# Kernel optimization log

Hardware: AMD Instinct MI355X
Metric: run time of the kernel (lower is better)

## Reference

```python
import jax, jax.numpy as jnp
import numpy as np

H = 12  # num_heads (init kwarg)


def setup_inputs() -> dict:
    key = jax.random.key(0)
    ks = jax.random.split(key, 9)
    B, S, D, M = 2, 1025, 768, 4
    hw = S - 1
    x = jax.random.normal(ks[0], (B, S, D), dtype=jnp.float32)
    masks = jax.random.randint(ks[1], (B, M, hw), 0, 2, dtype=jnp.int32)
    init = lambda k: jax.random.normal(k, (D, D), dtype=jnp.float32) * 0.02
    return {
        'x': x, 'masks': masks,
        'Wq': init(ks[2]), 'bq': jnp.zeros((D,), jnp.float32),
        'Wk': init(ks[3]), 'bk': jnp.zeros((D,), jnp.float32),
        'Wv': init(ks[4]), 'bv': jnp.zeros((D,), jnp.float32),
    }


def reference(x, masks, Wq, bq, Wk, bk, Wv, bv):
    B, S, D = x.shape
    hd = D // H
    scale = 1.0 / jnp.sqrt(jnp.asarray(hd, x.dtype))

    def heads(t):  # (B,S,D) -> (B,H,S,hd)
        return t.reshape(B, S, H, hd).transpose(0, 2, 1, 3)

    q = heads(x @ Wq.T + bq)
    k = heads(x @ Wk.T + bk)
    v = heads(x @ Wv.T + bv)

    scores_ori = jnp.einsum('bhqd,bhkd->bhqk', q, k) * scale  # (B,H,S,S)
    attn = jax.nn.softmax(scores_ori, axis=-1)  # dropout is identity at eval
    h = jnp.einsum('bhqk,bhkd->bhqd', attn, v)
    h = h.transpose(0, 2, 1, 3).reshape(B, S, D)

    # ---- mask-expanded attention (torch.no_grad branch) ----
    Mk, hw = masks.shape[1], masks.shape[2]
    m = masks.astype(x.dtype)  # (B,M,hw)
    # pad: position 0 (CLS) gets 0, positions 1..hw get the mask
    new_masks = jnp.pad(m, ((0, 0), (0, 0), (1, S - 1 - hw)))  # (B,M,S)
    bias = -10000.0 * (1.0 - new_masks)  # additive mask bias
    new_scores = scores_ori[:, None] + bias[:, :, None, None, :]  # (B,M,H,S,S)
    new_attn = jax.nn.softmax(new_scores, axis=-1)
    new_h = jnp.einsum('bmhqk,bhkd->bmhqd', new_attn, v)  # v repeated per mask
    new_h = new_h.transpose(0, 1, 3, 2, 4).reshape(B * Mk, S, D)

    img_idx = jnp.repeat(jnp.arange(B), Mk)  # [0]*M + [1]*M + ...
    new_x = jnp.broadcast_to(x[:, None], (B, Mk, S, D)).reshape(B * Mk, S, D)
    return (h, new_h, img_idx, new_x)
```

## Files before the change

### kernel.cpp

```cpp
#include <hip/hip_runtime.h>

typedef float f32x4 __attribute__((ext_vector_type(4)));
typedef short s16x8 __attribute__((ext_vector_type(8)));

constexpr int B  = 2;
constexpr int S  = 1025;
constexpr int D  = 768;
constexpr int DD = D * D;
constexpr int H  = 12;
constexpr int NM = 4;
constexpr int ROWS = B * S;
constexpr int BSD  = B * S * D;
constexpr int KPAD = 1088;
constexpr int NHB  = B * H;
constexpr int NQT  = 65;
constexpr int NKT  = 17;
constexpr int NV5  = 5;
constexpr int NATT = NHB * NQT;
constexpr int NCPY = 512;
constexpr int OUT_NEWH_OFF = BSD;
constexpr int OUT_IDX_OFF  = BSD + NM * BSD;
constexpr int OUT_NEWX_OFF = OUT_IDX_OFF + B * NM;

#define QSCALE 0.18033688011112042f

constexpr size_t QF_SZ = (size_t)NHB * NQT * 2 * 512;
constexpr size_t KF_SZ = (size_t)NHB * NKT * 4 * 2 * 512;
constexpr size_t VF_SZ = KF_SZ;

__device__ __forceinline__ unsigned short f2bf(float f) {
    unsigned u = __builtin_bit_cast(unsigned, f);
    u += 0x7FFF + ((u >> 16) & 1);
    return (unsigned short)(u >> 16);
}

__device__ __forceinline__ void gll16(const void* g, void* l) {
    __builtin_amdgcn_global_load_lds(
        (const __attribute__((address_space(1))) void*)g,
        (__attribute__((address_space(3))) void*)l, 16, 0, 0);
}

__global__ __launch_bounds__(256) void conv_kernel(
    const float* __restrict__ x, const float* __restrict__ Wq,
    const float* __restrict__ Wk, const float* __restrict__ Wv,
    const int* __restrict__ masks,
    unsigned short* __restrict__ xb, unsigned short* __restrict__ Wb,
    unsigned short* __restrict__ Mmb,
    unsigned short* __restrict__ Qf, unsigned short* __restrict__ Kf,
    unsigned short* __restrict__ Vf)
{
    constexpr int NX8 = BSD / 8;
    constexpr int NW8 = DD / 8;
    constexpr int TOT = NX8 + 3 * NW8;
    const int stride = gridDim.x * 256;
    const int tid = blockIdx.x * 256 + threadIdx.x;
    for (int c = tid; c < TOT; c += stride) {
        const float* src;
        unsigned short* dst;
        if (c < NX8) { src = x + (size_t)c * 8; dst = xb + (size_t)c * 8; }
        else {
            const int cc = c - NX8;
            const int mt = cc / NW8;
            const int rr = cc - mt * NW8;
            src = ((mt == 0) ? Wq : (mt == 1) ? Wk : Wv) + (size_t)rr * 8;
            dst = Wb + (size_t)mt * DD + (size_t)rr * 8;
        }
        const float4 a = *(const float4*)src;
        const float4 b2 = *(const float4*)(src + 4);
        s16x8 v;
        v[0] = (short)f2bf(a.x);  v[1] = (short)f2bf(a.y);
        v[2] = (short)f2bf(a.z);  v[3] = (short)f2bf(a.w);
        v[4] = (short)f2bf(b2.x); v[5] = (short)f2bf(b2.y);
        v[6] = (short)f2bf(b2.z); v[7] = (short)f2bf(b2.w);
        *(s16x8*)dst = v;
    }
    if (tid < B * NV5 * KPAD) {
        const int k    = tid % KPAD;
        const int rest = tid / KPAD;
        const int vv   = rest % NV5;
        const int bb   = rest / NV5;
        unsigned short m;
        if (vv == 0) m = (k < S) ? 0xFFFFu : 0u;
        else m = (k >= 1 && k < S &&
                  masks[(size_t)(bb * NM + vv - 1) * (S - 1) + k - 1]) ? 0xFFFFu : 0u;
        Mmb[tid] = m;
    }
    constexpr int KZ = NHB * 8 * 512;
    for (int i = tid; i < KZ; i += stride) {
        const int hb = i >> 12, off = i & 4095;
        Kf[(((size_t)(hb * NKT + NKT - 1)) << 12) + off] = 0;
        Vf[(((size_t)(hb * NKT + NKT - 1)) << 12) + off] = 0;
    }
    constexpr int QZ = NHB * 2 * 512;
    for (int i = tid; i < QZ; i += stride) {
        const int hb = i >> 10, off = i & 1023;
        Qf[(((size_t)(hb * NQT + NQT - 1) * 2) << 9) + off] = 0;
    }
}

__global__ __launch_bounds__(256, 2) void qkv_mfma_kernel(
    const unsigned short* __restrict__ xb, const unsigned short* __restrict__ Wb,
    const float* __restrict__ bq, const float* __restrict__ bk,
    const float* __restrict__ bv,
    unsigned short* __restrict__ Qf, unsigned short* __restrict__ Kf,
    unsigned short* __restrict__ Vf)
{
    __shared__ __align__(16) unsigned short Xs[2][64 * 64];
    __shared__ __align__(16) unsigned short Wl[2][64 * 64];

    const int t = threadIdx.x;
    const int row0 = blockIdx.x * 64;
    const int yy = blockIdx.y;
    const int mt = yy / 12;
    const int col0 = (yy % 12) * 64;
    const float* bias = (mt == 0) ? bq : (mt == 1) ? bk : bv;
    const unsigned short* Wsrc = Wb + (size_t)mt * DD;

    const int w = t >> 6, l = t & 63, lq = l & 15, grp = l >> 4;

    auto stage = [&](int buf, int k0) {
        #pragma unroll
        for (int i = 0; i < 2; ++i) {
            const int slot = i * 256 + t;
            const int r = slot >> 3, cl = slot & 7;
            const int cg = cl ^ (r & 7);
            int row = row0 + r; if (row > ROWS - 1) row = ROWS - 1;
            gll16(xb + (size_t)row * D + k0 + cg * 8, &Xs[buf][slot * 8]);
            gll16(Wsrc + (size_t)(col0 + r) * D + k0 + cg * 8, &Wl[buf][slot * 8]);
        }
    };

    f32x4 acc[4] = {};
    stage(0, 0);

    for (int ks = 0; ks < 12; ++ks) {
        const int cur = ks & 1;
        __syncthreads();
        if (ks + 1 < 12) stage(cur ^ 1, (ks + 1) * 64);

        s16x8 a[2];
        const int xr = w * 16 + lq;
        #pragma unroll
        for (int kh = 0; kh < 2; ++kh)
            a[kh] = *(const s16x8*)&Xs[cur][xr * 64 + (((kh * 4 + grp) ^ (xr & 7)) * 8)];
        #pragma unroll
        for (int nt = 0; nt < 4; ++nt) {
            const int wr = nt * 16 + lq;
            #pragma unroll
            for (int kh = 0; kh < 2; ++kh) {
                s16x8 bfr = *(const s16x8*)&Wl[cur][wr * 64 + (((kh * 4 + grp) ^ (wr & 7)) * 8)];
                acc[nt] = __builtin_amdgcn_mfma_f32_16x16x32_bf16(a[kh], bfr, acc[nt], 0, 0, 0);
            }
        }
    }

    #pragma unroll
    for (int nt = 0; nt < 4; ++nt) {
        const int col = col0 + nt * 16 + lq;
        const float bv_ = bias[col];
        #pragma unroll
        for (int r = 0; r < 4; ++r) {
            const int row = row0 + w * 16 + grp * 4 + r;
            if (row >= ROWS) continue;
            const float raw = acc[nt][r] + bv_;
            const int bb = (row >= S) ? 1 : 0;
            const int s  = row - bb * S;
            const int hb2 = bb * H + (col >> 6);
            const int d   = col & 63;
            if (mt == 0) {
                const size_t idx = (((size_t)(hb2 * NQT + (s >> 4)) * 2 + (d >> 5)) << 9)
                                 + (((((d >> 3) & 3) << 4) + (s & 15)) << 3) + (d & 7);
                Qf[idx] = f2bf(raw * QSCALE);
            } else if (mt == 1) {
                const size_t idx = ((((size_t)(hb2 * NKT + (s >> 6)) * 4 + ((s >> 4) & 3)) * 2 + (d >> 5)) << 9)
                                 + (((((d >> 3) & 3) << 4) + (s & 15)) << 3) + (d & 7);
                Kf[idx] = f2bf(raw);
            } else {
                const int kk = s & 63;
                const size_t idx = ((((size_t)(hb2 * NKT + (s >> 6)) * 4 + (d >> 4)) * 2 + (kk >> 5)) << 9)
                                 + (((((kk >> 3) & 3) << 4) + (d & 15)) << 3) + (kk & 7);
                Vf[idx] = f2bf(raw);
            }
        }
    }
}

__global__ __launch_bounds__(384) void attn_mfma_kernel(
    const unsigned short* __restrict__ Qf, const unsigned short* __restrict__ Kf,
    const unsigned short* __restrict__ Vf, const unsigned short* __restrict__ Mmb,
    const float* __restrict__ x,
    float* __restrict__ out_h, float* __restrict__ out_newh,
    float* __restrict__ out_newx, float* __restrict__ out_idx)
{
    if (blockIdx.x >= NATT) {
        const int cb = blockIdx.x - NATT;
        const int SLAB4  = S * D / 4;
        const int TOTAL4 = B * NM * SLAB4;
        const float4* x4 = (const float4*)x;
        float4* o4 = (float4*)out_newx;
        for (int f = cb * 384 + threadIdx.x; f < TOTAL4; f += NCPY * 384) {
            const int bm  = f / SLAB4;
            const int rem = f - bm * SLAB4;
            o4[f] = x4[(bm >> 2) * SLAB4 + rem];
        }
        if (cb == 0 && threadIdx.x < B * NM)
            out_idx[threadIdx.x] = (float)(threadIdx.x >> 2);
        return;
    }

    __shared__ __align__(16) unsigned short KVl[2][2][4096];
    __shared__ __align__(16) unsigned short Pb2[2][1024];

    const int orig = blockIdx.x;
    const int wgid = (orig & 7) * 195 + (orig >> 3);
    const int hb = wgid / NQT;
    const int qt = wgid - hb * NQT;
    const int b  = hb / H, hh = hb - b * H;
    const int q0 = qt * 16;

    const int t = threadIdx.x;
    const int w = t >> 6, l = t & 63;
    const int lq = l & 15, grp = l >> 4;

    const unsigned short* kfT = Kf + (((size_t)(hb * NKT)) << 12);
    const unsigned short* vfT = Vf + (((size_t)(hb * NKT)) << 12);

    auto stage = [&](int buf, int tile) {
        const unsigned short* ks = kfT + ((size_t)tile << 12);
        const unsigned short* vs = vfT + ((size_t)tile << 12);
        #pragma unroll
        for (int i = 0; i < 3; ++i) {
            const int s = t + i * 384;
            if (s < 512)       gll16(ks + s * 8, &KVl[buf][0][s * 8]);
            else if (s < 1024) gll16(vs + (s - 512) * 8, &KVl[buf][1][(s - 512) * 8]);
        }
    };

    stage(0, 0);

    if (w == 0) {
        s16x8 qf0, qf1;
        {
            const unsigned short* p = Qf + (((size_t)(hb * NQT + qt) * 2) << 9) + (l << 3);
            qf0 = *(const s16x8*)p;
            qf1 = *(const s16x8*)(p + 512);
        }
        #pragma unroll
        for (int it = 0; it < NKT; ++it) {
            const int cur = it & 1;
            __syncthreads();
            if (it + 1 < NKT) stage(cur ^ 1, it + 1);

            s16x8 kf[4][2];
            #pragma unroll
            for (int kt = 0; kt < 4; ++kt)
                #pragma unroll
                for (int kh = 0; kh < 2; ++kh)
                    kf[kt][kh] = *(const s16x8*)&KVl[cur][0][((kt * 2 + kh) << 9) + l * 8];

            f32x4 qk[4] = {};
            __builtin_amdgcn_s_setprio(1);
            #pragma unroll
            for (int kt = 0; kt < 4; ++kt) {
                qk[kt] = __builtin_amdgcn_mfma_f32_16x16x32_bf16(kf[kt][0], qf0, qk[kt], 0, 0, 0);
                qk[kt] = __builtin_amdgcn_mfma_f32_16x16x32_bf16(kf[kt][1], qf1, qk[kt], 0, 0, 0);
            }
            __builtin_amdgcn_s_setprio(0);

            unsigned short* P = &Pb2[cur][0];
            #pragma unroll
            for (int kt = 0; kt < 4; ++kt) {
                float e0, e1, e2, e3;
                asm("v_exp_f32 %0, %1" : "=v"(e0) : "v"(qk[kt][0]));
                asm("v_exp_f32 %0, %1" : "=v"(e1) : "v"(qk[kt][1]));
                asm("v_exp_f32 %0, %1" : "=v"(e2) : "v"(qk[kt][2]));
                asm("v_exp_f32 %0, %1" : "=v"(e3) : "v"(qk[kt][3]));
                unsigned d0, d1;
                asm("v_cvt_pk_bf16_f32 %0, %1, %2" : "=v"(d0) : "v"(e0), "v"(e1));
                asm("v_cvt_pk_bf16_f32 %0, %1, %2" : "=v"(d1) : "v"(e2), "v"(e3));
                const int chunk = kt * 2 + (grp >> 1);
                *(uint2*)&P[lq * 64 + ((chunk ^ (lq & 7)) * 8) + (grp & 1) * 4] =
                    make_uint2(d0, d1);
            }
        }
        __syncthreads();
    } else {
        const int vv = w - 1;
        const unsigned short* mbase = Mmb + (size_t)(b * NV5 + vv) * KPAD + grp * 8;

        s16x8 onesf;
        #pragma unroll
        for (int i = 0; i < 8; ++i) onesf[i] = (short)0x3F80;

        f32x4 acc[5] = {};
        s16x8 vfp[4][2];

        auto pv = [&](s16x8 ea0, s16x8 ea1, int mi) {
            s16x8 mm0 = *(const s16x8*)(mbase + mi * 64);
            s16x8 mm1 = *(const s16x8*)(mbase + mi * 64 + 32);
            s16x8 pa0 = ea0 & mm0;
            s16x8 pa1 = ea1 & mm1;
            __builtin_amdgcn_s_setprio(1);
            #pragma unroll
            for (int dt = 0; dt < 4; ++dt)
                acc[dt] = __builtin_amdgcn_mfma_f32_16x16x32_bf16(vfp[dt][0], pa0, acc[dt], 0, 0, 0);
            acc[4] = __builtin_amdgcn_mfma_f32_16x16x32_bf16(onesf, pa0, acc[4], 0, 0, 0);
            #pragma unroll
            for (int dt = 0; dt < 4; ++dt)
                acc[dt] = __builtin_amdgcn_mfma_f32_16x16x32_bf16(vfp[dt][1], pa1, acc[dt], 0, 0, 0);
            acc[4] = __builtin_amdgcn_mfma_f32_16x16x32_bf16(onesf, pa1, acc[4], 0, 0, 0);
            __builtin_amdgcn_s_setprio(0);
        };

        #pragma unroll
        for (int it = 0; it < NKT; ++it) {
            const int cur = it & 1;
            __syncthreads();
            if (it + 1 < NKT) stage(cur ^ 1, it + 1);

            s16x8 pr0, pr1;
            if (it > 0) {
                const unsigned short* Pr = &Pb2[cur ^ 1][0];
                pr0 = *(const s16x8*)&Pr[lq * 64 + ((grp ^ (lq & 7)) * 8)];
                pr1 = *(const s16x8*)&Pr[lq * 64 + (((4 + grp) ^ (lq & 7)) * 8)];
            }
            s16x8 vfc[4][2];
            #pragma unroll
            for (int dt = 0; dt < 4; ++dt)
                #pragma unroll
                for (int kh = 0; kh < 2; ++kh)
                    vfc[dt][kh] = *(const s16x8*)&KVl[cur][1][((dt * 2 + kh) << 9) + l * 8];

            if (it > 0) pv(pr0, pr1, it - 1);

            #pragma unroll
            for (int dt = 0; dt < 4; ++dt) {
                vfp[dt][0] = vfc[dt][0];
                vfp[dt][1] = vfc[dt][1];
            }
        }
        __syncthreads();
        {
            const unsigned short* Pr = &Pb2[(NKT - 1) & 1][0];
            s16x8 pr0 = *(const s16x8*)&Pr[lq * 64 + ((grp ^ (lq & 7)) * 8)];
            s16x8 pr1 = *(const s16x8*)&Pr[lq * 64 + (((4 + grp) ^ (lq & 7)) * 8)];
            pv(pr0, pr1, NKT - 1);
        }

        const int q = q0 + lq;
        if (q < S) {
            const float inv = 1.0f / acc[4][0];
            float* bp = ((vv == 0)
                ? out_h    + (size_t)(b * S + q) * D
                : out_newh + (size_t)((b * NM + vv - 1) * S + q) * D) + hh * 64 + grp * 4;
            #pragma unroll
            for (int dt = 0; dt < 4; ++dt) {
                float4 s4;
                s4.x = acc[dt][0] * inv; s4.y = acc[dt][1] * inv;
                s4.z = acc[dt][2] * inv; s4.w = acc[dt][3] * inv;
                *(float4*)(bp + dt * 16) = s4;
            }
        }
    }
}

extern "C" void kernel_launch(void* const* d_in, const int* in_sizes, int n_in,
                              void* d_out, int out_size, void* d_ws, size_t ws_size,
                              hipStream_t stream)
{
    const float* x     = (const float*)d_in[0];
    const int*   masks = (const int*)  d_in[1];
    const float* Wq    = (const float*)d_in[2];
    const float* bq    = (const float*)d_in[3];
    const float* Wk    = (const float*)d_in[4];
    const float* bk    = (const float*)d_in[5];
    const float* Wv    = (const float*)d_in[6];
    const float* bv    = (const float*)d_in[7];

    float* out = (float*)d_out;
    float* out_h    = out;
    float* out_newh = out + OUT_NEWH_OFF;
    float* out_idx  = out + OUT_IDX_OFF;
    float* out_newx = out + OUT_NEWX_OFF;

    unsigned short* Qf  = (unsigned short*)d_ws;
    unsigned short* Kf  = Qf + QF_SZ;
    unsigned short* Vf  = Kf + KF_SZ;
    unsigned short* Mmb = Vf + VF_SZ;

    unsigned short* xb = (unsigned short*)out_newx;
    unsigned short* Wb = xb + BSD;

    conv_kernel<<<1634, 256, 0, stream>>>(x, Wq, Wk, Wv, masks, xb, Wb, Mmb,
                                          Qf, Kf, Vf);
    {
        dim3 grid(33, 36);
        qkv_mfma_kernel<<<grid, 256, 0, stream>>>(xb, Wb, bq, bk, bv, Qf, Kf, Vf);
    }
    attn_mfma_kernel<<<NATT + NCPY, 384, 0, stream>>>(Qf, Kf, Vf, Mmb, x,
                                                      out_h, out_newh,
                                                      out_newx, out_idx);
}
```

Baseline: 96.81 us.

## Process two 16-row query tiles per workgroup to reuse staged K/V tiles

```diff
diff --git a/kernel.cpp b/kernel.cpp
--- a/kernel.cpp
+++ b/kernel.cpp
@@ -14,9 +14,10 @@
 constexpr int KPAD = 1088;
 constexpr int NHB  = B * H;
 constexpr int NQT  = 65;
+constexpr int NQB  = 33;
 constexpr int NKT  = 17;
 constexpr int NV5  = 5;
-constexpr int NATT = NHB * NQT;
+constexpr int NATT = NHB * NQB;
 constexpr int NCPY = 512;
 constexpr int OUT_NEWH_OFF = BSD;
 constexpr int OUT_IDX_OFF  = BSD + NM * BSD;
@@ -185,6 +186,24 @@
     }
 }
 
+__device__ __forceinline__ void pv_step(
+    f32x4 (&acc)[5], s16x8 ea0, s16x8 ea1, s16x8 mm0, s16x8 mm1,
+    const s16x8 (&vfp)[4][2], s16x8 onesf)
+{
+    s16x8 pa0 = ea0 & mm0;
+    s16x8 pa1 = ea1 & mm1;
+    __builtin_amdgcn_s_setprio(1);
+    #pragma unroll
+    for (int dt = 0; dt < 4; ++dt)
+        acc[dt] = __builtin_amdgcn_mfma_f32_16x16x32_bf16(vfp[dt][0], pa0, acc[dt], 0, 0, 0);
+    acc[4] = __builtin_amdgcn_mfma_f32_16x16x32_bf16(onesf, pa0, acc[4], 0, 0, 0);
+    #pragma unroll
+    for (int dt = 0; dt < 4; ++dt)
+        acc[dt] = __builtin_amdgcn_mfma_f32_16x16x32_bf16(vfp[dt][1], pa1, acc[dt], 0, 0, 0);
+    acc[4] = __builtin_amdgcn_mfma_f32_16x16x32_bf16(onesf, pa1, acc[4], 0, 0, 0);
+    __builtin_amdgcn_s_setprio(0);
+}
+
 __global__ __launch_bounds__(384) void attn_mfma_kernel(
     const unsigned short* __restrict__ Qf, const unsigned short* __restrict__ Kf,
     const unsigned short* __restrict__ Vf, const unsigned short* __restrict__ Mmb,
@@ -209,14 +228,14 @@
     }
 
     __shared__ __align__(16) unsigned short KVl[2][2][4096];
-    __shared__ __align__(16) unsigned short Pb2[2][1024];
+    __shared__ __align__(16) unsigned short Pb2[2][2][1024];
 
     const int orig = blockIdx.x;
-    const int wgid = (orig & 7) * 195 + (orig >> 3);
-    const int hb = wgid / NQT;
-    const int qt = wgid - hb * NQT;
+    const int wgid = (orig & 7) * 99 + (orig >> 3);
+    const int hb = wgid / NQB;
+    const int qt = wgid - hb * NQB;
     const int b  = hb / H, hh = hb - b * H;
-    const int q0 = qt * 16;
+    const int q0 = qt * 32;
 
     const int t = threadIdx.x;
     const int w = t >> 6, l = t & 63;
@@ -239,13 +258,14 @@
     stage(0, 0);
 
     if (w == 0) {
-        s16x8 qf0, qf1;
-        {
-            const unsigned short* p = Qf + (((size_t)(hb * NQT + qt) * 2) << 9) + (l << 3);
-            qf0 = *(const s16x8*)p;
-            qf1 = *(const s16x8*)(p + 512);
-        }
-        #pragma unroll
+        s16x8 qf[2][2];
+        #pragma unroll
+        for (int qs = 0; qs < 2; ++qs) {
+            int qtile = qt * 2 + qs; if (qtile > NQT - 1) qtile = NQT - 1;
+            const unsigned short* p = Qf + (((size_t)(hb * NQT + qtile) * 2) << 9) + (l << 3);
+            qf[qs][0] = *(const s16x8*)p;
+            qf[qs][1] = *(const s16x8*)(p + 512);
+        }
         for (int it = 0; it < NKT; ++it) {
             const int cur = it & 1;
             __syncthreads();
@@ -258,29 +278,32 @@
                 for (int kh = 0; kh < 2; ++kh)
                     kf[kt][kh] = *(const s16x8*)&KVl[cur][0][((kt * 2 + kh) << 9) + l * 8];
 
-            f32x4 qk[4] = {};
-            __builtin_amdgcn_s_setprio(1);
-            #pragma unroll
-            for (int kt = 0; kt < 4; ++kt) {
-                qk[kt] = __builtin_amdgcn_mfma_f32_16x16x32_bf16(kf[kt][0], qf0, qk[kt], 0, 0, 0);
-                qk[kt] = __builtin_amdgcn_mfma_f32_16x16x32_bf16(kf[kt][1], qf1, qk[kt], 0, 0, 0);
-            }
-            __builtin_amdgcn_s_setprio(0);
-
-            unsigned short* P = &Pb2[cur][0];
-            #pragma unroll
-            for (int kt = 0; kt < 4; ++kt) {
-                float e0, e1, e2, e3;
-                asm("v_exp_f32 %0, %1" : "=v"(e0) : "v"(qk[kt][0]));
-                asm("v_exp_f32 %0, %1" : "=v"(e1) : "v"(qk[kt][1]));
-                asm("v_exp_f32 %0, %1" : "=v"(e2) : "v"(qk[kt][2]));
-                asm("v_exp_f32 %0, %1" : "=v"(e3) : "v"(qk[kt][3]));
-                unsigned d0, d1;
-                asm("v_cvt_pk_bf16_f32 %0, %1, %2" : "=v"(d0) : "v"(e0), "v"(e1));
-                asm("v_cvt_pk_bf16_f32 %0, %1, %2" : "=v"(d1) : "v"(e2), "v"(e3));
-                const int chunk = kt * 2 + (grp >> 1);
-                *(uint2*)&P[lq * 64 + ((chunk ^ (lq & 7)) * 8) + (grp & 1) * 4] =
-                    make_uint2(d0, d1);
+            #pragma unroll
+            for (int qs = 0; qs < 2; ++qs) {
+                f32x4 qk[4] = {};
+                __builtin_amdgcn_s_setprio(1);
+                #pragma unroll
+                for (int kt = 0; kt < 4; ++kt) {
+                    qk[kt] = __builtin_amdgcn_mfma_f32_16x16x32_bf16(kf[kt][0], qf[qs][0], qk[kt], 0, 0, 0);
+                    qk[kt] = __builtin_amdgcn_mfma_f32_16x16x32_bf16(kf[kt][1], qf[qs][1], qk[kt], 0, 0, 0);
+                }
+                __builtin_amdgcn_s_setprio(0);
+
+                unsigned short* P = &Pb2[cur][qs][0];
+                #pragma unroll
+                for (int kt = 0; kt < 4; ++kt) {
+                    float e0, e1, e2, e3;
+                    asm("v_exp_f32 %0, %1" : "=v"(e0) : "v"(qk[kt][0]));
+                    asm("v_exp_f32 %0, %1" : "=v"(e1) : "v"(qk[kt][1]));
+                    asm("v_exp_f32 %0, %1" : "=v"(e2) : "v"(qk[kt][2]));
+                    asm("v_exp_f32 %0, %1" : "=v"(e3) : "v"(qk[kt][3]));
+                    unsigned d0, d1;
+                    asm("v_cvt_pk_bf16_f32 %0, %1, %2" : "=v"(d0) : "v"(e0), "v"(e1));
+                    asm("v_cvt_pk_bf16_f32 %0, %1, %2" : "=v"(d1) : "v"(e2), "v"(e3));
+                    const int chunk = kt * 2 + (grp >> 1);
+                    *(uint2*)&P[lq * 64 + ((chunk ^ (lq & 7)) * 8) + (grp & 1) * 4] =
+                        make_uint2(d0, d1);
+                }
             }
         }
         __syncthreads();
@@ -292,37 +315,23 @@
         #pragma unroll
         for (int i = 0; i < 8; ++i) onesf[i] = (short)0x3F80;
 
-        f32x4 acc[5] = {};
+        f32x4 acc0[5] = {};
+        f32x4 acc1[5] = {};
         s16x8 vfp[4][2];
 
-        auto pv = [&](s16x8 ea0, s16x8 ea1, int mi) {
-            s16x8 mm0 = *(const s16x8*)(mbase + mi * 64);
-            s16x8 mm1 = *(const s16x8*)(mbase + mi * 64 + 32);
-            s16x8 pa0 = ea0 & mm0;
-            s16x8 pa1 = ea1 & mm1;
-            __builtin_amdgcn_s_setprio(1);
-            #pragma unroll
-            for (int dt = 0; dt < 4; ++dt)
-                acc[dt] = __builtin_amdgcn_mfma_f32_16x16x32_bf16(vfp[dt][0], pa0, acc[dt], 0, 0, 0);
-            acc[4] = __builtin_amdgcn_mfma_f32_16x16x32_bf16(onesf, pa0, acc[4], 0, 0, 0);
-            #pragma unroll
-            for (int dt = 0; dt < 4; ++dt)
-                acc[dt] = __builtin_amdgcn_mfma_f32_16x16x32_bf16(vfp[dt][1], pa1, acc[dt], 0, 0, 0);
-            acc[4] = __builtin_amdgcn_mfma_f32_16x16x32_bf16(onesf, pa1, acc[4], 0, 0, 0);
-            __builtin_amdgcn_s_setprio(0);
-        };
-
-        #pragma unroll
         for (int it = 0; it < NKT; ++it) {
             const int cur = it & 1;
             __syncthreads();
             if (it + 1 < NKT) stage(cur ^ 1, it + 1);
 
-            s16x8 pr0, pr1;
+            s16x8 pr00, pr01, pr10, pr11;
             if (it > 0) {
-                const unsigned short* Pr = &Pb2[cur ^ 1][0];
-                pr0 = *(const s16x8*)&Pr[lq * 64 + ((grp ^ (lq & 7)) * 8)];
-                pr1 = *(const s16x8*)&Pr[lq * 64 + (((4 + grp) ^ (lq & 7)) * 8)];
+                const unsigned short* Pr0 = &Pb2[cur ^ 1][0][0];
+                const unsigned short* Pr1 = &Pb2[cur ^ 1][1][0];
+                pr00 = *(const s16x8*)&Pr0[lq * 64 + ((grp ^ (lq & 7)) * 8)];
+                pr01 = *(const s16x8*)&Pr0[lq * 64 + (((4 + grp) ^ (lq & 7)) * 8)];
+                pr10 = *(const s16x8*)&Pr1[lq * 64 + ((grp ^ (lq & 7)) * 8)];
+                pr11 = *(const s16x8*)&Pr1[lq * 64 + (((4 + grp) ^ (lq & 7)) * 8)];
             }
             s16x8 vfc[4][2];
             #pragma unroll
@@ -331,7 +340,13 @@
                 for (int kh = 0; kh < 2; ++kh)
                     vfc[dt][kh] = *(const s16x8*)&KVl[cur][1][((dt * 2 + kh) << 9) + l * 8];
 
-            if (it > 0) pv(pr0, pr1, it - 1);
+            if (it > 0) {
+                const int mi = it - 1;
+                s16x8 mm0 = *(const s16x8*)(mbase + mi * 64);
+                s16x8 mm1 = *(const s16x8*)(mbase + mi * 64 + 32);
+                pv_step(acc0, pr00, pr01, mm0, mm1, vfp, onesf);
+                pv_step(acc1, pr10, pr11, mm0, mm1, vfp, onesf);
+            }
 
             #pragma unroll
             for (int dt = 0; dt < 4; ++dt) {
@@ -341,14 +356,22 @@
         }
         __syncthreads();
         {
-            const unsigned short* Pr = &Pb2[(NKT - 1) & 1][0];
-            s16x8 pr0 = *(const s16x8*)&Pr[lq * 64 + ((grp ^ (lq & 7)) * 8)];
-            s16x8 pr1 = *(const s16x8*)&Pr[lq * 64 + (((4 + grp) ^ (lq & 7)) * 8)];
-            pv(pr0, pr1, NKT - 1);
-        }
-
-        const int q = q0 + lq;
-        if (q < S) {
+            const int mi = NKT - 1;
+            const unsigned short* Pr0 = &Pb2[mi & 1][0][0];
+            const unsigned short* Pr1 = &Pb2[mi & 1][1][0];
+            s16x8 pr00 = *(const s16x8*)&Pr0[lq * 64 + ((grp ^ (lq & 7)) * 8)];
+            s16x8 pr01 = *(const s16x8*)&Pr0[lq * 64 + (((4 + grp) ^ (lq & 7)) * 8)];
+            s16x8 pr10 = *(const s16x8*)&Pr1[lq * 64 + ((grp ^ (lq & 7)) * 8)];
+            s16x8 pr11 = *(const s16x8*)&Pr1[lq * 64 + (((4 + grp) ^ (lq & 7)) * 8)];
+            s16x8 mm0 = *(const s16x8*)(mbase + mi * 64);
+            s16x8 mm1 = *(const s16x8*)(mbase + mi * 64 + 32);
+            pv_step(acc0, pr00, pr01, mm0, mm1, vfp, onesf);
+            pv_step(acc1, pr10, pr11, mm0, mm1, vfp, onesf);
+        }
+
+        auto store_q = [&](f32x4 (&acc)[5], int qs) {
+            const int q = q0 + qs * 16 + lq;
+            if (q >= S) return;
             const float inv = 1.0f / acc[4][0];
             float* bp = ((vv == 0)
                 ? out_h    + (size_t)(b * S + q) * D
@@ -360,7 +383,9 @@
                 s4.z = acc[dt][2] * inv; s4.w = acc[dt][3] * inv;
                 *(float4*)(bp + dt * 16) = s4;
             }
-        }
+        };
+        store_q(acc0, 0);
+        store_q(acc1, 1);
     }
 }
 
```

After: 112.3 us. 1.16x slower.

## Load K/V fragments directly from global into registers instead of LDS staging

Applied to the files above, without the earlier changes.

```diff
diff --git a/kernel.cpp b/kernel.cpp
--- a/kernel.cpp
+++ b/kernel.cpp
@@ -185,6 +185,24 @@
     }
 }
 
+__device__ __forceinline__ void pv_step(
+    f32x4 (&acc)[5], s16x8 ea0, s16x8 ea1, s16x8 mm0, s16x8 mm1,
+    const s16x8 (&vfp)[4][2], s16x8 onesf)
+{
+    s16x8 pa0 = ea0 & mm0;
+    s16x8 pa1 = ea1 & mm1;
+    __builtin_amdgcn_s_setprio(1);
+    #pragma unroll
+    for (int dt = 0; dt < 4; ++dt)
+        acc[dt] = __builtin_amdgcn_mfma_f32_16x16x32_bf16(vfp[dt][0], pa0, acc[dt], 0, 0, 0);
+    acc[4] = __builtin_amdgcn_mfma_f32_16x16x32_bf16(onesf, pa0, acc[4], 0, 0, 0);
+    #pragma unroll
+    for (int dt = 0; dt < 4; ++dt)
+        acc[dt] = __builtin_amdgcn_mfma_f32_16x16x32_bf16(vfp[dt][1], pa1, acc[dt], 0, 0, 0);
+    acc[4] = __builtin_amdgcn_mfma_f32_16x16x32_bf16(onesf, pa1, acc[4], 0, 0, 0);
+    __builtin_amdgcn_s_setprio(0);
+}
+
 __global__ __launch_bounds__(384) void attn_mfma_kernel(
     const unsigned short* __restrict__ Qf, const unsigned short* __restrict__ Kf,
     const unsigned short* __restrict__ Vf, const unsigned short* __restrict__ Mmb,
@@ -208,7 +226,6 @@
         return;
     }
 
-    __shared__ __align__(16) unsigned short KVl[2][2][4096];
     __shared__ __align__(16) unsigned short Pb2[2][1024];
 
     const int orig = blockIdx.x;
@@ -222,22 +239,6 @@
     const int w = t >> 6, l = t & 63;
     const int lq = l & 15, grp = l >> 4;
 
-    const unsigned short* kfT = Kf + (((size_t)(hb * NKT)) << 12);
-    const unsigned short* vfT = Vf + (((size_t)(hb * NKT)) << 12);
-
-    auto stage = [&](int buf, int tile) {
-        const unsigned short* ks = kfT + ((size_t)tile << 12);
-        const unsigned short* vs = vfT + ((size_t)tile << 12);
-        #pragma unroll
-        for (int i = 0; i < 3; ++i) {
-            const int s = t + i * 384;
-            if (s < 512)       gll16(ks + s * 8, &KVl[buf][0][s * 8]);
-            else if (s < 1024) gll16(vs + (s - 512) * 8, &KVl[buf][1][(s - 512) * 8]);
-        }
-    };
-
-    stage(0, 0);
-
     if (w == 0) {
         s16x8 qf0, qf1;
         {
@@ -245,18 +246,19 @@
             qf0 = *(const s16x8*)p;
             qf1 = *(const s16x8*)(p + 512);
         }
-        #pragma unroll
-        for (int it = 0; it < NKT; ++it) {
-            const int cur = it & 1;
-            __syncthreads();
-            if (it + 1 < NKT) stage(cur ^ 1, it + 1);
-
-            s16x8 kf[4][2];
+        const unsigned short* kfb = Kf + (((size_t)(hb * NKT)) << 12) + (l << 3);
+        s16x8 kf[4][2];
+        auto load_k = [&](int tile) {
             #pragma unroll
             for (int kt = 0; kt < 4; ++kt)
                 #pragma unroll
                 for (int kh = 0; kh < 2; ++kh)
-                    kf[kt][kh] = *(const s16x8*)&KVl[cur][0][((kt * 2 + kh) << 9) + l * 8];
+                    kf[kt][kh] = *(const s16x8*)&kfb[((size_t)(tile * 8 + kt * 2 + kh)) << 9];
+        };
+        load_k(0);
+
+        for (int it = 0; it < NKT; ++it) {
+            __syncthreads();
 
             f32x4 qk[4] = {};
             __builtin_amdgcn_s_setprio(1);
@@ -267,7 +269,9 @@
             }
             __builtin_amdgcn_s_setprio(0);
 
-            unsigned short* P = &Pb2[cur][0];
+            if (it + 1 < NKT) load_k(it + 1);
+
+            unsigned short* P = &Pb2[it & 1][0];
             #pragma unroll
             for (int kt = 0; kt < 4; ++kt) {
                 float e0, e1, e2, e3;
@@ -287,64 +291,55 @@
     } else {
         const int vv = w - 1;
         const unsigned short* mbase = Mmb + (size_t)(b * NV5 + vv) * KPAD + grp * 8;
+        const unsigned short* vfb = Vf + (((size_t)(hb * NKT)) << 12) + (l << 3);
 
         s16x8 onesf;
         #pragma unroll
         for (int i = 0; i < 8; ++i) onesf[i] = (short)0x3F80;
 
         f32x4 acc[5] = {};
-        s16x8 vfp[4][2];
-
-        auto pv = [&](s16x8 ea0, s16x8 ea1, int mi) {
-            s16x8 mm0 = *(const s16x8*)(mbase + mi * 64);
-            s16x8 mm1 = *(const s16x8*)(mbase + mi * 64 + 32);
-            s16x8 pa0 = ea0 & mm0;
-            s16x8 pa1 = ea1 & mm1;
-            __builtin_amdgcn_s_setprio(1);
-            #pragma unroll
-            for (int dt = 0; dt < 4; ++dt)
-                acc[dt] = __builtin_amdgcn_mfma_f32_16x16x32_bf16(vfp[dt][0], pa0, acc[dt], 0, 0, 0);
-            acc[4] = __builtin_amdgcn_mfma_f32_16x16x32_bf16(onesf, pa0, acc[4], 0, 0, 0);
-            #pragma unroll
-            for (int dt = 0; dt < 4; ++dt)
-                acc[dt] = __builtin_amdgcn_mfma_f32_16x16x32_bf16(vfp[dt][1], pa1, acc[dt], 0, 0, 0);
-            acc[4] = __builtin_amdgcn_mfma_f32_16x16x32_bf16(onesf, pa1, acc[4], 0, 0, 0);
-            __builtin_amdgcn_s_setprio(0);
-        };
-
-        #pragma unroll
-        for (int it = 0; it < NKT; ++it) {
-            const int cur = it & 1;
-            __syncthreads();
-            if (it + 1 < NKT) stage(cur ^ 1, it + 1);
-
-            s16x8 pr0, pr1;
-            if (it > 0) {
-                const unsigned short* Pr = &Pb2[cur ^ 1][0];
-                pr0 = *(const s16x8*)&Pr[lq * 64 + ((grp ^ (lq & 7)) * 8)];
-                pr1 = *(const s16x8*)&Pr[lq * 64 + (((4 + grp) ^ (lq & 7)) * 8)];
-            }
-            s16x8 vfc[4][2];
+        s16x8 vA[4][2], vB[4][2];
+
+        auto load_v = [&](s16x8 (&dst)[4][2], int tile) {
             #pragma unroll
             for (int dt = 0; dt < 4; ++dt)
                 #pragma unroll
                 for (int kh = 0; kh < 2; ++kh)
-                    vfc[dt][kh] = *(const s16x8*)&KVl[cur][1][((dt * 2 + kh) << 9) + l * 8];
-
-            if (it > 0) pv(pr0, pr1, it - 1);
+                    dst[dt][kh] = *(const s16x8*)&vfb[((size_t)(tile * 8 + dt * 2 + kh)) << 9];
+        };
+
+        load_v(vA, 0);
+        __syncthreads();
+
+        for (int it = 1; it < NKT; ++it) {
+            __syncthreads();
+
+            const unsigned short* Pr = &Pb2[(it - 1) & 1][0];
+            s16x8 pr0 = *(const s16x8*)&Pr[lq * 64 + ((grp ^ (lq & 7)) * 8)];
+            s16x8 pr1 = *(const s16x8*)&Pr[lq * 64 + (((4 + grp) ^ (lq & 7)) * 8)];
+
+            load_v(vB, it);
+
+            const int mi = it - 1;
+            s16x8 mm0 = *(const s16x8*)(mbase + mi * 64);
+            s16x8 mm1 = *(const s16x8*)(mbase + mi * 64 + 32);
+            pv_step(acc, pr0, pr1, mm0, mm1, vA, onesf);
 
             #pragma unroll
             for (int dt = 0; dt < 4; ++dt) {
-                vfp[dt][0] = vfc[dt][0];
-                vfp[dt][1] = vfc[dt][1];
+                vA[dt][0] = vB[dt][0];
+                vA[dt][1] = vB[dt][1];
             }
         }
         __syncthreads();
         {
-            const unsigned short* Pr = &Pb2[(NKT - 1) & 1][0];
+            const int mi = NKT - 1;
+            const unsigned short* Pr = &Pb2[mi & 1][0];
             s16x8 pr0 = *(const s16x8*)&Pr[lq * 64 + ((grp ^ (lq & 7)) * 8)];
             s16x8 pr1 = *(const s16x8*)&Pr[lq * 64 + (((4 + grp) ^ (lq & 7)) * 8)];
-            pv(pr0, pr1, NKT - 1);
+            s16x8 mm0 = *(const s16x8*)(mbase + mi * 64);
+            s16x8 mm1 = *(const s16x8*)(mbase + mi * 64 + 32);
+            pv_step(acc, pr0, pr1, mm0, mm1, vA, onesf);
         }
 
         const int q = q0 + lq;
```

Result: slower. 107.7 us (+11.2%).
